# Kernel tuning notes

Hardware: AMD Instinct MI355X
Metric: run time of the kernel (lower is better)

Reference implementation:

```python
import jax, jax.numpy as jnp
import numpy as np

PATCH = 64      # patch generator patch size
LD = 1.0        # self.ld
WS = 11         # SSIM gaussian window size
SIGMA = 1.5
C1 = 0.01 ** 2
C2 = 0.03 ** 2


def _gauss_window(channels):
    x = jnp.arange(WS, dtype=jnp.float32)
    g = jnp.exp(-((x - WS // 2) ** 2) / (2.0 * SIGMA * SIGMA))
    g = g / g.sum()
    w2 = jnp.outer(g, g)               # (WS, WS), sums to 1
    return jnp.broadcast_to(w2[None, None], (channels, 1, WS, WS))


def _dwconv(x, w, channels):
    # depthwise 'same' conv, padding = WS//2 (matches F.conv2d(..., padding=ws//2, groups=C))
    p = WS // 2
    return jax.lax.conv_general_dilated(
        x, w, window_strides=(1, 1), padding=[(p, p), (p, p)],
        dimension_numbers=("NCHW", "OIHW", "NCHW"), feature_group_count=channels)


def _ssim(img1, img2):
    # img1, img2: (n, C, h, w) -> per-image mean SSIM, shape (n,)
    ch = img1.shape[1]
    w = _gauss_window(ch).astype(img1.dtype)
    mu1 = _dwconv(img1, w, ch)
    mu2 = _dwconv(img2, w, ch)
    mu1_sq, mu2_sq, mu1_mu2 = mu1 * mu1, mu2 * mu2, mu1 * mu2
    sigma1_sq = _dwconv(img1 * img1, w, ch) - mu1_sq
    sigma2_sq = _dwconv(img2 * img2, w, ch) - mu2_sq
    sigma12 = _dwconv(img1 * img2, w, ch) - mu1_mu2
    ssim_map = ((2.0 * mu1_mu2 + C1) * (2.0 * sigma12 + C2)) / (
        (mu1_sq + mu2_sq + C1) * (sigma1_sq + sigma2_sq + C2))
    return jnp.mean(ssim_map, axis=(1, 2, 3))


def _to_patches(x, ps):
    # (B, C, H, W) -> (B, P, C, ps, ps) with P = (H//ps)*(W//ps)
    B, C, H, W = x.shape
    x = x.reshape(B, C, H // ps, ps, W // ps, ps)
    x = x.transpose(0, 2, 4, 1, 3, 5)
    return x.reshape(B, (H // ps) * (W // ps), C, ps, ps)


def setup_inputs() -> dict:
    key = jax.random.key(0)
    ks = jax.random.split(key, 5)
    shp = (32, 3, 512, 512)
    names = ["A", "N", "GT", "G", "BG"]
    return {n: jax.random.uniform(k, shp, dtype=jnp.float32) for n, k in zip(names, ks)}


def reference(A, N, GT, G, BG):
    pA = _to_patches(A, PATCH)
    pN = _to_patches(N, PATCH)
    pGT = _to_patches(GT, PATCH)
    pG = _to_patches(G, PATCH)
    pBG = _to_patches(BG, PATCH)
    B, P, C, h, w = pA.shape
    # batched SSIM over all (B*P) patches (replaces the python double loop)
    ssim_scores = _ssim(pN.reshape(B * P, C, h, w), pGT.reshape(B * P, C, h, w)).reshape(B, P)
    diff = jnp.minimum(LD * (1.0 - ssim_scores), jnp.ones_like(ssim_scores))
    bg_loss = jnp.mean((pBG - pG) ** 2, axis=(2, 3, 4))
    a_loss = jnp.mean((pA - pG) ** 2, axis=(2, 3, 4))
    loss = diff * bg_loss + (1.0 - diff) * a_loss
    return jnp.sum(loss)
```

## Files before the change

### kernel.cpp

```cpp
#include <hip/hip_runtime.h>
#include <math.h>

#define C1C 1e-4f
#define C2C 9e-4f

#define GW0 0.00102838f
#define GW1 0.00759876f
#define GW2 0.03600077f
#define GW3 0.10936069f
#define GW4 0.21300554f
#define GW5 0.26601173f
__device__ __forceinline__ float conv11(const float* w) {
    float a = GW0 * (w[0] + w[10]);
    a = fmaf(GW1, w[1] + w[9], a);
    a = fmaf(GW2, w[2] + w[8], a);
    a = fmaf(GW3, w[3] + w[7], a);
    a = fmaf(GW4, w[4] + w[6], a);
    a = fmaf(GW5, w[5], a);
    return a;
}

#define SROWS 74
#define SSTR  36

__global__ __launch_bounds__(256, 3) void ssim_fused_kernel(
    const float* __restrict__ A,  const float* __restrict__ Nimg,
    const float* __restrict__ GT, const float* __restrict__ G,
    const float* __restrict__ BG,
    float* __restrict__ ssim_sum, float* __restrict__ sa_sum,
    float* __restrict__ sbg_sum)
{
    __shared__ float S0[SROWS][SSTR];
    __shared__ float S1[SROWS][SSTR];
    __shared__ float S2[SROWS][SSTR];

    const int q  = blockIdx.x;
    const int c  = blockIdx.y;
    const int b  = q >> 6;
    const int pp = q & 63;
    const int ph = pp >> 3;
    const int pw = pp & 7;
    const size_t base = ((size_t)(b * 3 + c) << 18)
                      + ((size_t)(ph * 64) << 9)
                      + (size_t)(pw * 64);
    const int t = threadIdx.x;

    for (int i = t; i < 10 * SSTR; i += 256) {
        const int r  = i / SSTR;
        const int cc = i - r * SSTR;
        const int rr = (r < 5) ? r : 64 + r;
        S0[rr][cc] = 0.f; S1[rr][cc] = 0.f; S2[rr][cc] = 0.f;
    }

    const int hr   = t >> 2;
    const int hseg = t & 3;
    const int c0   = hseg << 3;
    const size_t rowBase = base + ((size_t)hr << 9);
    const int vcol = t & 31;
    const int vr0  = (t >> 5) << 3;

    float accS = 0.f;

    for (int h = 0; h < 2; ++h) {
        const int g0 = (h << 5) + c0;
        float xs[18], ys[18];
        #pragma unroll
        for (int m = 0; m < 6; ++m) {
            const int cb = g0 - 8 + 4 * m;
            float4 xv = make_float4(0.f, 0.f, 0.f, 0.f);
            float4 yv = make_float4(0.f, 0.f, 0.f, 0.f);
            if (cb >= 0 && cb < 64) {
                xv = *(const float4*)(Nimg + rowBase + cb);
                yv = *(const float4*)(GT   + rowBase + cb);
            }
            #pragma unroll
            for (int u = 0; u < 4; ++u) {
                const int j = 4 * m + u - 3;
                if (j >= 0 && j < 18) {
                    xs[j] = (&xv.x)[u];
                    ys[j] = (&yv.x)[u];
                }
            }
        }

        float hx[8], hy[8];
        {
            float p[18];
            #pragma unroll
            for (int i = 0; i < 18; ++i) p[i] = xs[i] * ys[i];
            #pragma unroll
            for (int mm = 0; mm < 2; ++mm) {
                float4 o;
                #pragma unroll
                for (int u = 0; u < 4; ++u) (&o.x)[u] = conv11(&p[4*mm + u]);
                *(float4*)&S2[5 + hr][c0 + 4*mm] = o;
            }
            #pragma unroll
            for (int i = 0; i < 18; ++i) p[i] = xs[i] * xs[i];
            #pragma unroll
            for (int mm = 0; mm < 2; ++mm) {
                float4 o;
                #pragma unroll
                for (int u = 0; u < 4; ++u) (&o.x)[u] = conv11(&p[4*mm + u]);
                *(float4*)&S0[5 + hr][c0 + 4*mm] = o;
            }
            #pragma unroll
            for (int i = 0; i < 18; ++i) p[i] = ys[i] * ys[i];
            #pragma unroll
            for (int mm = 0; mm < 2; ++mm) {
                float4 o;
                #pragma unroll
                for (int u = 0; u < 4; ++u) (&o.x)[u] = conv11(&p[4*mm + u]);
                *(float4*)&S1[5 + hr][c0 + 4*mm] = o;
            }
            #pragma unroll
            for (int o = 0; o < 8; ++o) hx[o] = conv11(&xs[o]);
            #pragma unroll
            for (int o = 0; o < 8; ++o) hy[o] = conv11(&ys[o]);
        }
        __syncthreads();

        float Exx[8], Eyy[8], Exy[8];
        {
            float w[18];
            #pragma unroll
            for (int d = 0; d < 18; ++d) w[d] = S0[vr0 + d][vcol];
            #pragma unroll
            for (int o = 0; o < 8; ++o) Exx[o] = conv11(&w[o]);
            #pragma unroll
            for (int d = 0; d < 18; ++d) w[d] = S1[vr0 + d][vcol];
            #pragma unroll
            for (int o = 0; o < 8; ++o) Eyy[o] = conv11(&w[o]);
            #pragma unroll
            for (int d = 0; d < 18; ++d) w[d] = S2[vr0 + d][vcol];
            #pragma unroll
            for (int o = 0; o < 8; ++o) Exy[o] = conv11(&w[o]);
        }
        __syncthreads();

        #pragma unroll
        for (int mm = 0; mm < 2; ++mm) {
            float4 o0, o1;
            #pragma unroll
            for (int u = 0; u < 4; ++u) {
                (&o0.x)[u] = hx[4*mm + u];
                (&o1.x)[u] = hy[4*mm + u];
            }
            *(float4*)&S0[5 + hr][c0 + 4*mm] = o0;
            *(float4*)&S1[5 + hr][c0 + 4*mm] = o1;
        }
        __syncthreads();

        {
            float w[18];
            #pragma unroll
            for (int d = 0; d < 18; ++d) w[d] = S0[vr0 + d][vcol];
            float mu1[8];
            #pragma unroll
            for (int o = 0; o < 8; ++o) mu1[o] = conv11(&w[o]);
            #pragma unroll
            for (int d = 0; d < 18; ++d) w[d] = S1[vr0 + d][vcol];
            #pragma unroll
            for (int o = 0; o < 8; ++o) {
                const float m2  = conv11(&w[o]);
                const float m1  = mu1[o];
                const float m1s = m1 * m1, m2s = m2 * m2, m12 = m1 * m2;
                const float s1  = Exx[o] - m1s;
                const float s2v = Eyy[o] - m2s;
                const float s12 = Exy[o] - m12;
                const float num = (2.f * m12 + C1C) * (2.f * s12 + C2C);
                const float den = (m1s + m2s + C1C) * (s1 + s2v + C2C);
                accS += num / den;
            }
        }
        __syncthreads();
    }

    float sa = 0.f, sbg = 0.f;
    #pragma unroll
    for (int it = 0; it < 4; ++it) {
        const int idx  = t + 256 * it;
        const int row  = idx >> 4;
        const int col4 = (idx & 15) << 2;
        const size_t off = base + ((size_t)row << 9) + col4;
        const float4 av  = *(const float4*)(A  + off);
        const float4 gv  = *(const float4*)(G  + off);
        const float4 bgv = *(const float4*)(BG + off);
        float d0 = bgv.x - gv.x, d1 = bgv.y - gv.y, d2 = bgv.z - gv.z, d3 = bgv.w - gv.w;
        sbg += d0*d0 + d1*d1 + d2*d2 + d3*d3;
        float e0 = av.x - gv.x, e1 = av.y - gv.y, e2 = av.z - gv.z, e3 = av.w - gv.w;
        sa  += e0*e0 + e1*e1 + e2*e2 + e3*e3;
    }

    #pragma unroll
    for (int off = 32; off; off >>= 1) {
        accS += __shfl_down(accS, off, 64);
        sa   += __shfl_down(sa,   off, 64);
        sbg  += __shfl_down(sbg,  off, 64);
    }
    const int wv = t >> 6;
    if ((t & 63) == 0) {
        S0[0][wv] = accS; S0[1][wv] = sa; S0[2][wv] = sbg;
    }
    __syncthreads();
    if (t == 0) {
        const int plane = q * 3 + c;
        ssim_sum[plane] = S0[0][0] + S0[0][1] + S0[0][2] + S0[0][3];
        sa_sum[plane]   = S0[1][0] + S0[1][1] + S0[1][2] + S0[1][3];
        sbg_sum[plane]  = S0[2][0] + S0[2][1] + S0[2][2] + S0[2][3];
    }
}

__global__ __launch_bounds__(256) void combine_kernel(
    const float* __restrict__ ssim_sum, const float* __restrict__ sa_sum,
    const float* __restrict__ sbg_sum, float* __restrict__ out)
{
    __shared__ float red[4];
    const int t = threadIdx.x;
    const float invN = 1.f / 12288.f;
    float acc = 0.f;
    #pragma unroll
    for (int r = 0; r < 8; ++r) {
        const int qq = t + 256 * r;
        const float ss = ssim_sum[3*qq] + ssim_sum[3*qq+1] + ssim_sum[3*qq+2];
        const float sa = sa_sum[3*qq]   + sa_sum[3*qq+1]   + sa_sum[3*qq+2];
        const float sb = sbg_sum[3*qq]  + sbg_sum[3*qq+1]  + sbg_sum[3*qq+2];
        const float ssim = ss * invN;
        const float diff = fminf(1.f - ssim, 1.f);
        acc += diff * (sb * invN) + (1.f - diff) * (sa * invN);
    }
    #pragma unroll
    for (int off = 32; off; off >>= 1) acc += __shfl_down(acc, off, 64);
    if ((t & 63) == 0) red[t >> 6] = acc;
    __syncthreads();
    if (t == 0) out[0] = red[0] + red[1] + red[2] + red[3];
}

extern "C" void kernel_launch(void* const* d_in, const int* in_sizes, int n_in,
                              void* d_out, int out_size, void* d_ws, size_t ws_size,
                              hipStream_t stream) {
    const float* A  = (const float*)d_in[0];
    const float* Nn = (const float*)d_in[1];
    const float* GT = (const float*)d_in[2];
    const float* G  = (const float*)d_in[3];
    const float* BG = (const float*)d_in[4];
    float* out      = (float*)d_out;

    float* ssim_sum = (float*)d_ws;
    float* sa_sum   = ssim_sum + 6144;
    float* sbg_sum  = ssim_sum + 12288;

    ssim_fused_kernel<<<dim3(2048, 3), 256, 0, stream>>>(
        A, Nn, GT, G, BG, ssim_sum, sa_sum, sbg_sum);
    combine_kernel<<<1, 256, 0, stream>>>(ssim_sum, sa_sum, sbg_sum, out);
}
```

Baseline: 445.3 us.

## Stage all five horizontal conv results in LDS to drop two barriers per half

```diff
diff --git a/kernel.cpp b/kernel.cpp
--- a/kernel.cpp
+++ b/kernel.cpp
@@ -33,6 +33,8 @@
     __shared__ float S0[SROWS][SSTR];
     __shared__ float S1[SROWS][SSTR];
     __shared__ float S2[SROWS][SSTR];
+    __shared__ float S3[SROWS][SSTR];
+    __shared__ float S4[SROWS][SSTR];
 
     const int q  = blockIdx.x;
     const int c  = blockIdx.y;
@@ -40,9 +42,9 @@
     const int pp = q & 63;
     const int ph = pp >> 3;
     const int pw = pp & 7;
-    const size_t base = ((size_t)(b * 3 + c) << 18)
-                      + ((size_t)(ph * 64) << 9)
-                      + (size_t)(pw * 64);
+    const unsigned base = ((unsigned)(b * 3 + c) << 18)
+                        + ((unsigned)(ph * 64) << 9)
+                        + (unsigned)(pw * 64);
     const int t = threadIdx.x;
 
     for (int i = t; i < 10 * SSTR; i += 256) {
@@ -50,12 +52,13 @@
         const int cc = i - r * SSTR;
         const int rr = (r < 5) ? r : 64 + r;
         S0[rr][cc] = 0.f; S1[rr][cc] = 0.f; S2[rr][cc] = 0.f;
+        S3[rr][cc] = 0.f; S4[rr][cc] = 0.f;
     }
 
     const int hr   = t >> 2;
     const int hseg = t & 3;
     const int c0   = hseg << 3;
-    const size_t rowBase = base + ((size_t)hr << 9);
+    const unsigned rowBase = base + ((unsigned)hr << 9);
     const int vcol = t & 31;
     const int vr0  = (t >> 5) << 3;
 
@@ -83,7 +86,6 @@
             }
         }
 
-        float hx[8], hy[8];
         {
             float p[18];
             #pragma unroll
@@ -114,14 +116,21 @@
                 *(float4*)&S1[5 + hr][c0 + 4*mm] = o;
             }
             #pragma unroll
-            for (int o = 0; o < 8; ++o) hx[o] = conv11(&xs[o]);
-            #pragma unroll
-            for (int o = 0; o < 8; ++o) hy[o] = conv11(&ys[o]);
+            for (int mm = 0; mm < 2; ++mm) {
+                float4 o0, o1;
+                #pragma unroll
+                for (int u = 0; u < 4; ++u) {
+                    (&o0.x)[u] = conv11(&xs[4*mm + u]);
+                    (&o1.x)[u] = conv11(&ys[4*mm + u]);
+                }
+                *(float4*)&S3[5 + hr][c0 + 4*mm] = o0;
+                *(float4*)&S4[5 + hr][c0 + 4*mm] = o1;
+            }
         }
         __syncthreads();
 
-        float Exx[8], Eyy[8], Exy[8];
         {
+            float Exx[8], Eyy[8], Exy[8], mu1[8];
             float w[18];
             #pragma unroll
             for (int d = 0; d < 18; ++d) w[d] = S0[vr0 + d][vcol];
@@ -135,31 +144,12 @@
             for (int d = 0; d < 18; ++d) w[d] = S2[vr0 + d][vcol];
             #pragma unroll
             for (int o = 0; o < 8; ++o) Exy[o] = conv11(&w[o]);
-        }
-        __syncthreads();
-
-        #pragma unroll
-        for (int mm = 0; mm < 2; ++mm) {
-            float4 o0, o1;
-            #pragma unroll
-            for (int u = 0; u < 4; ++u) {
-                (&o0.x)[u] = hx[4*mm + u];
-                (&o1.x)[u] = hy[4*mm + u];
-            }
-            *(float4*)&S0[5 + hr][c0 + 4*mm] = o0;
-            *(float4*)&S1[5 + hr][c0 + 4*mm] = o1;
-        }
-        __syncthreads();
-
-        {
-            float w[18];
-            #pragma unroll
-            for (int d = 0; d < 18; ++d) w[d] = S0[vr0 + d][vcol];
-            float mu1[8];
+            #pragma unroll
+            for (int d = 0; d < 18; ++d) w[d] = S3[vr0 + d][vcol];
             #pragma unroll
             for (int o = 0; o < 8; ++o) mu1[o] = conv11(&w[o]);
             #pragma unroll
-            for (int d = 0; d < 18; ++d) w[d] = S1[vr0 + d][vcol];
+            for (int d = 0; d < 18; ++d) w[d] = S4[vr0 + d][vcol];
             #pragma unroll
             for (int o = 0; o < 8; ++o) {
                 const float m2  = conv11(&w[o]);
@@ -182,7 +172,7 @@
         const int idx  = t + 256 * it;
         const int row  = idx >> 4;
         const int col4 = (idx & 15) << 2;
-        const size_t off = base + ((size_t)row << 9) + col4;
+        const unsigned off = base + ((unsigned)row << 9) + col4;
         const float4 av  = *(const float4*)(A  + off);
         const float4 gv  = *(const float4*)(G  + off);
         const float4 bgv = *(const float4*)(BG + off);
```

Result: no change. 444.6 us (-0.2%).
